# Optimization experiments

Hardware: AMD Instinct MI355X
Metric: run time of the kernel (lower is better)

## Reference

```python
import jax, jax.numpy as jnp
import numpy as np

TAU = 20.0        # LIFNeuron default tau
THRESHOLD = 1.0   # LIFNeuron default threshold
RESET = 0.0       # LIFNeuron default reset
DT = 1.0          # SpikingNeuralNetwork dt
ALPHA = DT / TAU

B, T, I, H, O = 256, 128, 512, 1024, 512


def setup_inputs() -> dict:
    key = jax.random.key(0)
    ks = jax.random.split(key, 6)
    def w(k, shape, fan_in):
        return (jax.random.normal(k, shape, jnp.float32) / np.sqrt(fan_in)).astype(jnp.float32)
    return {
        "x":  jax.random.normal(ks[0], (B, T, I), jnp.float32),
        "We": w(ks[1], (I, H), I), "be": jnp.zeros((H,), jnp.float32),
        "W1": w(ks[2], (H, H), H), "b1": jnp.zeros((H,), jnp.float32),
        "W2": w(ks[3], (H, H), H), "b2": jnp.zeros((H,), jnp.float32),
        "Wo": w(ks[4], (H, O), H), "bo": jnp.zeros((O,), jnp.float32),
    }


def _lif(v, inp):
    # v += (-v + inp) * dt/tau; spike = (v >= thr); v = v*(1-spike) + reset*spike
    v = v + (inp - v) * ALPHA
    spike = (v >= THRESHOLD).astype(v.dtype)
    v = v * (1.0 - spike) + RESET * spike
    return v, spike


def reference(x, We, be, W1, b1, W2, b2, Wo, bo):
    b, t, _ = x.shape
    h_dim = We.shape[1]
    o_dim = Wo.shape[1]

    def step(carry, xt):
        v1, v2, vo = carry
        h = jax.nn.relu(xt @ We + be)          # [B, H]
        v1, s1 = _lif(v1, h)                   # neuron 0 (only 2 of 3 neurons used: zip truncation)
        h = s1 @ W1 + b1
        v2, s2 = _lif(v2, h)                   # neuron 1
        h = s2 @ W2 + b2                       # last hidden layer: no neuron applied before output_layer
        vo, so = _lif(vo, h @ Wo + bo)         # output neuron
        return (v1, v2, vo), (s1, s2, so)

    init = (jnp.zeros((b, h_dim), x.dtype),
            jnp.zeros((b, h_dim), x.dtype),
            jnp.zeros((b, o_dim), x.dtype))
    _, (S1, S2, SO) = jax.lax.scan(step, init, jnp.swapaxes(x, 0, 1))  # time-major scan
    # output_spike at last timestep + full (detached) spike history, stacked over time
    return SO[-1], S1, S2, SO
```

## Files before the change

kernel.cpp:

```cpp
#include <hip/hip_runtime.h>
#include <cstdint>
#include <cstddef>

#define B_ 256
#define T_ 128
#define I_ 512
#define H_ 1024
#define O_ 512
static constexpr float ALPHA = 1.0f / 20.0f;
static constexpr float THR   = 1.0f;
static constexpr float S12   = 0.000244140625f;

typedef _Float16 f16;
typedef __attribute__((ext_vector_type(8))) _Float16 f16x8;
typedef __attribute__((ext_vector_type(4))) float f32x4;

__device__ inline void gload_lds16(const void* gsrc, void* ldsdst) {
    __builtin_amdgcn_global_load_lds(
        (const __attribute__((address_space(1))) unsigned int*)gsrc,
        (__attribute__((address_space(3))) unsigned int*)ldsdst, 16, 0, 0);
}

template<bool PERM_X, bool RELU>
__global__ __launch_bounds__(256)
void gemm128(const float* __restrict__ A, const float* __restrict__ Bw,
             const float* __restrict__ bias, float* __restrict__ C,
             int M, int N, int K) {
    constexpr int BM = 128, BN = 128, BK = 16, TM = 8, TN = 8;
    __shared__ float As[BK][BM];
    __shared__ float Bs[BK][BN + 4];

    const int tid = threadIdx.x;
    const int ntile = N / BN;
    const int bx = blockIdx.x % ntile;
    const int by = blockIdx.x / ntile;
    const int row0 = by * BM, col0 = bx * BN;
    const int tx = tid & 15;
    const int ty = tid >> 4;

    float acc[TM][TN] = {};

    for (int k0 = 0; k0 < K; k0 += BK) {
#pragma unroll
        for (int p = 0; p < 2; ++p) {
            int f = tid + p * 256;
            int r  = f >> 2;
            int kc = (f & 3) << 2;
            int m = row0 + r;
            const float* arow;
            if (PERM_X) {
                int t = m >> 8;
                int b = m & 255;
                arow = A + (size_t)(b * T_ + t) * K;
            } else {
                arow = A + (size_t)m * K;
            }
            float4 v = *reinterpret_cast<const float4*>(arow + k0 + kc);
            As[kc + 0][r] = v.x;
            As[kc + 1][r] = v.y;
            As[kc + 2][r] = v.z;
            As[kc + 3][r] = v.w;
        }
#pragma unroll
        for (int p = 0; p < 2; ++p) {
            int f = tid + p * 256;
            int r  = f >> 5;
            int nc = (f & 31) << 2;
            float4 v = *reinterpret_cast<const float4*>(Bw + (size_t)(k0 + r) * N + col0 + nc);
            *reinterpret_cast<float4*>(&Bs[r][nc]) = v;
        }
        __syncthreads();

#pragma unroll
        for (int k = 0; k < BK; ++k) {
            float a[TM], b[TN];
#pragma unroll
            for (int i = 0; i < TM; ++i) a[i] = As[k][ty * TM + i];
#pragma unroll
            for (int j = 0; j < TN; ++j) b[j] = Bs[k][tx * TN + j];
#pragma unroll
            for (int i = 0; i < TM; ++i)
#pragma unroll
                for (int j = 0; j < TN; ++j)
                    acc[i][j] += a[i] * b[j];
        }
        __syncthreads();
    }

#pragma unroll
    for (int i = 0; i < TM; ++i) {
        size_t m = (size_t)(row0 + ty * TM + i);
#pragma unroll
        for (int jj = 0; jj < TN; jj += 4) {
            int n = col0 + tx * TN + jj;
            float4 c4;
            float c0 = acc[i][jj + 0] + bias[n + 0];
            float c1 = acc[i][jj + 1] + bias[n + 1];
            float c2 = acc[i][jj + 2] + bias[n + 2];
            float c3 = acc[i][jj + 3] + bias[n + 3];
            if (RELU) {
                c0 = fmaxf(c0, 0.f); c1 = fmaxf(c1, 0.f);
                c2 = fmaxf(c2, 0.f); c3 = fmaxf(c3, 0.f);
            }
            c4.x = c0; c4.y = c1; c4.z = c2; c4.w = c3;
            *reinterpret_cast<float4*>(C + m * N + n) = c4;
        }
    }
}

template<bool SPLITX, bool PERM, bool RELU, bool WRITE_LAST>
__global__ __launch_bounds__(256, 2)
void gemm_lif(const float* __restrict__ A,
              const f16* __restrict__ Bhi, const f16* __restrict__ Blo,
              const float* __restrict__ bias,
              float* __restrict__ S, float* __restrict__ last_out,
              int N, int K) {
    constexpr int BK = 32;
    constexpr int NBUF = SPLITX ? 4 : 3;
    constexpr int BUFSTR = NBUF * 4096;
    constexpr size_t SMEM = (2 * BUFSTR * 2 > 64 * 132 * 4)
                                ? (size_t)(2 * BUFSTR * 2)
                                : (size_t)(64 * 132 * 4);
    __shared__ __align__(16) char smem[SMEM];
    f16* sm = (f16*)smem;
    float (*Cs)[132] = (float (*)[132])smem;

    const int tid  = threadIdx.x;
    const int lane = tid & 63;
    const int w    = tid >> 6;
    const int wr   = w >> 1, wc = w & 1;
    const int ntile = N >> 7;
    const int bx = blockIdx.x % ntile;
    const int b  = blockIdx.x / ntile;
    const int col0 = bx << 7;

    f32x4 acc0[4][4], acc1[4][4];
#pragma unroll
    for (int mi = 0; mi < 4; ++mi)
#pragma unroll
        for (int ni = 0; ni < 4; ++ni) {
            acc0[mi][ni] = {0.f, 0.f, 0.f, 0.f};
            acc1[mi][ni] = {0.f, 0.f, 0.f, 0.f};
        }

    {
        f16* Ah0 = sm;
        f16* Bh0 = sm + 4096;
        f16* Bl0 = sm + 8192;
        f16* Al0 = sm + 12288;
#pragma unroll
        for (int p = 0; p < 2; ++p) {
            int chunk = w * 2 + p;
            int r  = chunk * 16 + (lane >> 2);
            int kq = lane & 3;
            size_t off = (size_t)(col0 + r) * K + kq * 8;
            gload_lds16(Bhi + off, Bh0 + chunk * 512);
            gload_lds16(Blo + off, Bl0 + chunk * 512);
        }
#pragma unroll
        for (int p = 0; p < 4; ++p) {
            int c = tid + p * 256;
            int r = c >> 3;
            int q = c & 7;
            const float* arow = PERM ? A + (size_t)(b * T_ + r) * K
                                     : A + (size_t)(r * B_ + b) * K;
            float4 v = *reinterpret_cast<const float4*>(arow + q * 4);
            union { f16 h[4]; uint2 u; } hi;
            hi.h[0] = (f16)v.x; hi.h[1] = (f16)v.y;
            hi.h[2] = (f16)v.z; hi.h[3] = (f16)v.w;
            *reinterpret_cast<uint2*>(&Ah0[r * BK + q * 4]) = hi.u;
            if (SPLITX) {
                union { f16 h[4]; uint2 u; } lo;
                lo.h[0] = (f16)((v.x - (float)hi.h[0]) * 4096.0f);
                lo.h[1] = (f16)((v.y - (float)hi.h[1]) * 4096.0f);
                lo.h[2] = (f16)((v.z - (float)hi.h[2]) * 4096.0f);
                lo.h[3] = (f16)((v.w - (float)hi.h[3]) * 4096.0f);
                *reinterpret_cast<uint2*>(&Al0[r * BK + q * 4]) = lo.u;
            }
        }
    }
    __syncthreads();

    const int NIT = K / BK;
    for (int it = 0; it < NIT; ++it) {
        const int cur = it & 1, nxt = cur ^ 1;
        const bool more = (it + 1 < NIT);
        const int k0n = (it + 1) * BK;

        f16* Ah_c = sm + cur * BUFSTR;
        f16* Bh_c = Ah_c + 4096;
        f16* Bl_c = Ah_c + 8192;
        f16* Al_c = Ah_c + 12288;
        f16* Ah_n = sm + nxt * BUFSTR;
        f16* Bh_n = Ah_n + 4096;
        f16* Bl_n = Ah_n + 8192;
        f16* Al_n = Ah_n + 12288;

        float4 a4[4];
        if (more) {
#pragma unroll
            for (int p = 0; p < 2; ++p) {
                int chunk = w * 2 + p;
                int r  = chunk * 16 + (lane >> 2);
                int kq = lane & 3;
                size_t off = (size_t)(col0 + r) * K + k0n + kq * 8;
                gload_lds16(Bhi + off, Bh_n + chunk * 512);
                gload_lds16(Blo + off, Bl_n + chunk * 512);
            }
#pragma unroll
            for (int p = 0; p < 4; ++p) {
                int c = tid + p * 256;
                int r = c >> 3;
                int q = c & 7;
                const float* arow = PERM ? A + (size_t)(b * T_ + r) * K
                                         : A + (size_t)(r * B_ + b) * K;
                a4[p] = *reinterpret_cast<const float4*>(arow + k0n + q * 4);
            }
        }

        {
            f16x8 ahi[4], alo[4];
#pragma unroll
            for (int mi = 0; mi < 4; ++mi) {
                int ar = (wr * 64 + mi * 16 + (lane & 15)) * BK + (lane >> 4) * 8;
                ahi[mi] = *reinterpret_cast<const f16x8*>(&Ah_c[ar]);
                if (SPLITX) alo[mi] = *reinterpret_cast<const f16x8*>(&Al_c[ar]);
            }
#pragma unroll
            for (int ni = 0; ni < 4; ++ni) {
                int br = (wc * 64 + ni * 16 + (lane & 15)) * BK + (lane >> 4) * 8;
                f16x8 bh = *reinterpret_cast<const f16x8*>(&Bh_c[br]);
                f16x8 bl = *reinterpret_cast<const f16x8*>(&Bl_c[br]);
#pragma unroll
                for (int mi = 0; mi < 4; ++mi) {
                    acc0[mi][ni] = __builtin_amdgcn_mfma_f32_16x16x32_f16(
                        ahi[mi], bh, acc0[mi][ni], 0, 0, 0);
                    acc1[mi][ni] = __builtin_amdgcn_mfma_f32_16x16x32_f16(
                        ahi[mi], bl, acc1[mi][ni], 0, 0, 0);
                    if (SPLITX)
                        acc1[mi][ni] = __builtin_amdgcn_mfma_f32_16x16x32_f16(
                            alo[mi], bh, acc1[mi][ni], 0, 0, 0);
                }
            }
        }

        if (more) {
#pragma unroll
            for (int p = 0; p < 4; ++p) {
                int c = tid + p * 256;
                int r = c >> 3;
                int q = c & 7;
                float4 v = a4[p];
                union { f16 h[4]; uint2 u; } hi;
                hi.h[0] = (f16)v.x; hi.h[1] = (f16)v.y;
                hi.h[2] = (f16)v.z; hi.h[3] = (f16)v.w;
                *reinterpret_cast<uint2*>(&Ah_n[r * BK + q * 4]) = hi.u;
                if (SPLITX) {
                    union { f16 h[4]; uint2 u; } lo;
                    lo.h[0] = (f16)((v.x - (float)hi.h[0]) * 4096.0f);
                    lo.h[1] = (f16)((v.y - (float)hi.h[1]) * 4096.0f);
                    lo.h[2] = (f16)((v.z - (float)hi.h[2]) * 4096.0f);
                    lo.h[3] = (f16)((v.w - (float)hi.h[3]) * 4096.0f);
                    *reinterpret_cast<uint2*>(&Al_n[r * BK + q * 4]) = lo.u;
                }
            }
        }
        __syncthreads();
    }

    float v = 0.f, s = 0.f;
    float* Sp = S + (size_t)b * N + col0 + (tid & 127);
    const size_t tstride = (size_t)B_ * N;

    if (wr == 0) {
#pragma unroll
        for (int ni = 0; ni < 4; ++ni) {
            int col = wc * 64 + ni * 16 + (lane & 15);
            float bv = bias[col0 + col];
#pragma unroll
            for (int mi = 0; mi < 4; ++mi) {
                int rowb = mi * 16 + ((lane >> 4) << 2);
#pragma unroll
                for (int r = 0; r < 4; ++r) {
                    float cv = acc0[mi][ni][r] + S12 * acc1[mi][ni][r] + bv;
                    if (RELU) cv = fmaxf(cv, 0.f);
                    Cs[rowb + r][col] = cv;
                }
            }
        }
    }
    __syncthreads();
    if (tid < 128) {
#pragma unroll 4
        for (int t = 0; t < 64; ++t) {
            float in = Cs[t][tid];
            v = v + (in - v) * ALPHA;
            bool sp = (v >= THR);
            s = sp ? 1.0f : 0.0f;
            Sp[(size_t)t * tstride] = s;
            v = sp ? 0.0f : v;
        }
    }
    __syncthreads();
    if (wr == 1) {
#pragma unroll
        for (int ni = 0; ni < 4; ++ni) {
            int col = wc * 64 + ni * 16 + (lane & 15);
            float bv = bias[col0 + col];
#pragma unroll
            for (int mi = 0; mi < 4; ++mi) {
                int rowb = mi * 16 + ((lane >> 4) << 2);
#pragma unroll
                for (int r = 0; r < 4; ++r) {
                    float cv = acc0[mi][ni][r] + S12 * acc1[mi][ni][r] + bv;
                    if (RELU) cv = fmaxf(cv, 0.f);
                    Cs[rowb + r][col] = cv;
                }
            }
        }
    }
    __syncthreads();
    if (tid < 128) {
#pragma unroll 4
        for (int t = 64; t < 128; ++t) {
            float in = Cs[t - 64][tid];
            v = v + (in - v) * ALPHA;
            bool sp = (v >= THR);
            s = sp ? 1.0f : 0.0f;
            Sp[(size_t)t * tstride] = s;
            v = sp ? 0.0f : v;
        }
        if (WRITE_LAST) last_out[(size_t)b * N + col0 + tid] = s;
    }
}

__global__ __launch_bounds__(256, 2)
void gemm_lif_x(const float* __restrict__ A,
                const f16* __restrict__ Bhi, const f16* __restrict__ Blo,
                const float* __restrict__ bias,
                float* __restrict__ S,
                uint32_t* __restrict__ Pk,
                int N, int K) {
    constexpr int BK = 32;
    constexpr int BUFSTR = 4 * 4096;
    __shared__ __align__(16) char smem[2 * BUFSTR * 2];
    f16* sm = (f16*)smem;
    float (*Cs)[132] = (float (*)[132])smem;

    const int tid  = threadIdx.x;
    const int lane = tid & 63;
    const int w    = tid >> 6;
    const int wr   = w >> 1, wc = w & 1;
    const int nt   = N >> 7;
    const int ls   = 31 - __builtin_clz(nt);
    const int jj_  = blockIdx.x >> 3;
    const int bx   = jj_ & (nt - 1);
    const int b    = ((blockIdx.x & 7) << 5) + (jj_ >> ls);
    const int col0 = bx << 7;
    const int sw = (((lane >> 4) ^ ((lane >> 1) & 3)) << 3);

    f32x4 acc0[4][4], acc1[4][4];
#pragma unroll
    for (int mi = 0; mi < 4; ++mi)
#pragma unroll
        for (int ni = 0; ni < 4; ++ni) {
            acc0[mi][ni] = {0.f, 0.f, 0.f, 0.f};
            acc1[mi][ni] = {0.f, 0.f, 0.f, 0.f};
        }

    {
        f16* Ah0 = sm;
        f16* Bh0 = sm + 4096;
        f16* Bl0 = sm + 8192;
        f16* Al0 = sm + 12288;
#pragma unroll
        for (int p = 0; p < 2; ++p) {
            int chunk = w * 2 + p;
            int r  = chunk * 16 + (lane >> 2);
            int kq = lane & 3;
            size_t off = (size_t)(col0 + r) * K + kq * 8;
            gload_lds16(Bhi + off, Bh0 + chunk * 512);
            gload_lds16(Blo + off, Bl0 + chunk * 512);
        }
#pragma unroll
        for (int p = 0; p < 4; ++p) {
            int c = tid + p * 256;
            int r = c >> 3;
            int q = c & 7;
            const float* arow = A + (size_t)(b * T_ + r) * K;
            float4 v = *reinterpret_cast<const float4*>(arow + q * 4);
            int aoff = r * 32 + ((((q >> 1) ^ ((r >> 1) & 3))) << 3) + ((q & 1) << 2);
            union { f16 h[4]; uint2 u; } hi;
            hi.h[0] = (f16)v.x; hi.h[1] = (f16)v.y;
            hi.h[2] = (f16)v.z; hi.h[3] = (f16)v.w;
            *reinterpret_cast<uint2*>(&Ah0[aoff]) = hi.u;
            union { f16 h[4]; uint2 u; } lo;
            lo.h[0] = (f16)((v.x - (float)hi.h[0]) * 4096.0f);
            lo.h[1] = (f16)((v.y - (float)hi.h[1]) * 4096.0f);
            lo.h[2] = (f16)((v.z - (float)hi.h[2]) * 4096.0f);
            lo.h[3] = (f16)((v.w - (float)hi.h[3]) * 4096.0f);
            *reinterpret_cast<uint2*>(&Al0[aoff]) = lo.u;
        }
    }
    __syncthreads();

    const int NIT = K / BK;
    for (int it = 0; it < NIT; ++it) {
        const int cur = it & 1, nxt = cur ^ 1;
        const bool more = (it + 1 < NIT);
        const int k0n = (it + 1) * BK;

        f16* Ah_c = sm + cur * BUFSTR;
        f16* Bh_c = Ah_c + 4096;
        f16* Bl_c = Ah_c + 8192;
        f16* Al_c = Ah_c + 12288;
        f16* Ah_n = sm + nxt * BUFSTR;
        f16* Bh_n = Ah_n + 4096;
        f16* Bl_n = Ah_n + 8192;
        f16* Al_n = Ah_n + 12288;

        float4 a4[4];
        if (more) {
#pragma unroll
            for (int p = 0; p < 2; ++p) {
                int chunk = w * 2 + p;
                int r  = chunk * 16 + (lane >> 2);
                int kq = lane & 3;
                size_t off = (size_t)(col0 + r) * K + k0n + kq * 8;
                gload_lds16(Bhi + off, Bh_n + chunk * 512);
                gload_lds16(Blo + off, Bl_n + chunk * 512);
            }
#pragma unroll
            for (int p = 0; p < 4; ++p) {
                int c = tid + p * 256;
                int r = c >> 3;
                int q = c & 7;
                const float* arow = A + (size_t)(b * T_ + r) * K;
                a4[p] = *reinterpret_cast<const float4*>(arow + k0n + q * 4);
            }
        }

        {
            f16x8 ahi[4], alo[4];
#pragma unroll
            for (int mi = 0; mi < 4; ++mi) {
                int ar = (wr * 64 + mi * 16 + (lane & 15)) * 32 + sw;
                ahi[mi] = *reinterpret_cast<const f16x8*>(&Ah_c[ar]);
                alo[mi] = *reinterpret_cast<const f16x8*>(&Al_c[ar]);
            }
#pragma unroll
            for (int ni = 0; ni < 4; ++ni) {
                int br = (wc * 64 + ni * 16 + (lane & 15)) * 32 + sw;
                f16x8 bh = *reinterpret_cast<const f16x8*>(&Bh_c[br]);
                f16x8 bl = *reinterpret_cast<const f16x8*>(&Bl_c[br]);
#pragma unroll
                for (int mi = 0; mi < 4; ++mi) {
                    acc0[mi][ni] = __builtin_amdgcn_mfma_f32_16x16x32_f16(
                        ahi[mi], bh, acc0[mi][ni], 0, 0, 0);
                    acc1[mi][ni] = __builtin_amdgcn_mfma_f32_16x16x32_f16(
                        ahi[mi], bl, acc1[mi][ni], 0, 0, 0);
                    acc1[mi][ni] = __builtin_amdgcn_mfma_f32_16x16x32_f16(
                        alo[mi], bh, acc1[mi][ni], 0, 0, 0);
                }
            }
        }

        if (more) {
#pragma unroll
            for (int p = 0; p < 4; ++p) {
                int c = tid + p * 256;
                int r = c >> 3;
                int q = c & 7;
                float4 v = a4[p];
                int aoff = r * 32 + ((((q >> 1) ^ ((r >> 1) & 3))) << 3) + ((q & 1) << 2);
                union { f16 h[4]; uint2 u; } hi;
                hi.h[0] = (f16)v.x; hi.h[1] = (f16)v.y;
                hi.h[2] = (f16)v.z; hi.h[3] = (f16)v.w;
                *reinterpret_cast<uint2*>(&Ah_n[aoff]) = hi.u;
                union { f16 h[4]; uint2 u; } lo;
                lo.h[0] = (f16)((v.x - (float)hi.h[0]) * 4096.0f);
                lo.h[1] = (f16)((v.y - (float)hi.h[1]) * 4096.0f);
                lo.h[2] = (f16)((v.z - (float)hi.h[2]) * 4096.0f);
                lo.h[3] = (f16)((v.w - (float)hi.h[3]) * 4096.0f);
                *reinterpret_cast<uint2*>(&Al_n[aoff]) = lo.u;
            }
        }
        __syncthreads();
    }

    float v = 0.f;
    float* Sp = S + (size_t)b * N + col0 + (tid & 127);
    const size_t tstride = (size_t)B_ * N;
    const int PkW = N >> 5;
    const size_t pkbase = (size_t)(col0 >> 5) + ((tid >> 6) << 1);

    if (wr == 0) {
#pragma unroll
        for (int ni = 0; ni < 4; ++ni) {
            int col = wc * 64 + ni * 16 + (lane & 15);
            float bv = bias[col0 + col];
#pragma unroll
            for (int mi = 0; mi < 4; ++mi) {
                int rowb = mi * 16 + ((lane >> 4) << 2);
#pragma unroll
                for (int r = 0; r < 4; ++r) {
                    float cv = fmaxf(acc0[mi][ni][r] + S12 * acc1[mi][ni][r] + bv, 0.f);
                    Cs[rowb + r][col] = cv;
                }
            }
        }
    }
    __syncthreads();
    if (tid < 128) {
#pragma unroll 4
        for (int t = 0; t < 64; ++t) {
            float in = Cs[t][tid];
            v = v + (in - v) * ALPHA;
            bool sp = (v >= THR);
            Sp[(size_t)t * tstride] = sp ? 1.0f : 0.0f;
            v = sp ? 0.0f : v;
            unsigned long long bm = __ballot(sp);
            if (lane == 0)
                *reinterpret_cast<unsigned long long*>(
                    &Pk[((size_t)t * B_ + b) * PkW + pkbase]) = bm;
        }
    }
    __syncthreads();
    if (wr == 1) {
#pragma unroll
        for (int ni = 0; ni < 4; ++ni) {
            int col = wc * 64 + ni * 16 + (lane & 15);
            float bv = bias[col0 + col];
#pragma unroll
            for (int mi = 0; mi < 4; ++mi) {
                int rowb = mi * 16 + ((lane >> 4) << 2);
#pragma unroll
                for (int r = 0; r < 4; ++r) {
                    float cv = fmaxf(acc0[mi][ni][r] + S12 * acc1[mi][ni][r] + bv, 0.f);
                    Cs[rowb + r][col] = cv;
                }
            }
        }
    }
    __syncthreads();
    if (tid < 128) {
#pragma unroll 4
        for (int t = 64; t < 128; ++t) {
            float in = Cs[t - 64][tid];
            v = v + (in - v) * ALPHA;
            bool sp = (v >= THR);
            Sp[(size_t)t * tstride] = sp ? 1.0f : 0.0f;
            v = sp ? 0.0f : v;
            unsigned long long bm = __ballot(sp);
            if (lane == 0)
                *reinterpret_cast<unsigned long long*>(
                    &Pk[((size_t)t * B_ + b) * PkW + pkbase]) = bm;
        }
    }
}

template<bool WRITE_LAST, bool PACK_OUT>
__global__ __launch_bounds__(256, 2)
void gemm_lif_pk(const uint32_t* __restrict__ Apk,
                 const f16* __restrict__ Bhi, const f16* __restrict__ Blo,
                 const float* __restrict__ bias,
                 float* __restrict__ S,
                 float* __restrict__ last_out,
                 uint32_t* __restrict__ Pk_out,
                 int N, int K) {
    __shared__ __align__(16) char smem[64 * 132 * 4];
    f16* sm = (f16*)smem;
    float (*Cs)[132] = (float (*)[132])smem;

    const int tid  = threadIdx.x;
    const int lane = tid & 63;
    const int w    = tid >> 6;
    const int wr   = w >> 1, wc = w & 1;
    const int nt   = N >> 7;
    const int ls   = 31 - __builtin_clz(nt);
    const int jj_  = blockIdx.x >> 3;
    const int bx   = jj_ & (nt - 1);
    const int b    = ((blockIdx.x & 7) << 5) + (jj_ >> ls);
    const int col0 = bx << 7;
    const int sw = (((lane >> 4) ^ ((lane >> 1) & 3)) << 3);
    const int PkW = K >> 5;
    const int sh  = (lane >> 4) << 3;

    size_t arow[4];
#pragma unroll
    for (int mi = 0; mi < 4; ++mi) {
        int r = wr * 64 + mi * 16 + (lane & 15);
        arow[mi] = ((size_t)r * B_ + b) * PkW;
    }

    f32x4 acc0[4][4], acc1[4][4];
#pragma unroll
    for (int mi = 0; mi < 4; ++mi)
#pragma unroll
        for (int ni = 0; ni < 4; ++ni) {
            acc0[mi][ni] = {0.f, 0.f, 0.f, 0.f};
            acc1[mi][ni] = {0.f, 0.f, 0.f, 0.f};
        }

    {
#pragma unroll
        for (int p = 0; p < 2; ++p) {
            int chunk = w * 2 + p;
            int r  = chunk * 16 + (lane >> 2);
            int kq = lane & 3;
            size_t off = (size_t)(col0 + r) * K + kq * 8;
            gload_lds16(Bhi + off, sm + chunk * 512);
            gload_lds16(Blo + off, sm + 4096 + chunk * 512);
        }
    }
    __syncthreads();

    const int NIT = K / 32;
    for (int it = 0; it < NIT; ++it) {
        const int cur = it & 1, nxt = cur ^ 1;
        f16* Bh_c = sm + cur * 8192;
        f16* Bl_c = Bh_c + 4096;
        if (it + 1 < NIT) {
            f16* Bh_n = sm + nxt * 8192;
            f16* Bl_n = Bh_n + 4096;
            int k0n = (it + 1) * 32;
#pragma unroll
            for (int p = 0; p < 2; ++p) {
                int chunk = w * 2 + p;
                int r  = chunk * 16 + (lane >> 2);
                int kq = lane & 3;
                size_t off = (size_t)(col0 + r) * K + k0n + kq * 8;
                gload_lds16(Bhi + off, Bh_n + chunk * 512);
                gload_lds16(Blo + off, Bl_n + chunk * 512);
            }
        }

        f16x8 af[4];
#pragma unroll
        for (int mi = 0; mi < 4; ++mi) {
            uint32_t mm = Apk[arow[mi] + it] >> sh;
            union { f16 h[8]; f16x8 v; } au;
#pragma unroll
            for (int j = 0; j < 8; ++j)
                au.h[j] = ((mm >> j) & 1) ? (f16)1.0f : (f16)0.0f;
            af[mi] = au.v;
        }

#pragma unroll
        for (int ni = 0; ni < 4; ++ni) {
            int br = (wc * 64 + ni * 16 + (lane & 15)) * 32 + sw;
            f16x8 bh = *reinterpret_cast<const f16x8*>(&Bh_c[br]);
            f16x8 bl = *reinterpret_cast<const f16x8*>(&Bl_c[br]);
#pragma unroll
            for (int mi = 0; mi < 4; ++mi) {
                acc0[mi][ni] = __builtin_amdgcn_mfma_f32_16x16x32_f16(
                    af[mi], bh, acc0[mi][ni], 0, 0, 0);
                acc1[mi][ni] = __builtin_amdgcn_mfma_f32_16x16x32_f16(
                    af[mi], bl, acc1[mi][ni], 0, 0, 0);
            }
        }
        __syncthreads();
    }

    float v = 0.f, s = 0.f;
    float* Sp = S + (size_t)b * N + col0 + (tid & 127);
    const size_t tstride = (size_t)B_ * N;
    const int PkWo = N >> 5;
    const size_t pkbase = (size_t)(col0 >> 5) + ((tid >> 6) << 1);

    if (wr == 0) {
#pragma unroll
        for (int ni = 0; ni < 4; ++ni) {
            int col = wc * 64 + ni * 16 + (lane & 15);
            float bv = bias[col0 + col];
#pragma unroll
            for (int mi = 0; mi < 4; ++mi) {
                int rowb = mi * 16 + ((lane >> 4) << 2);
#pragma unroll
                for (int r = 0; r < 4; ++r)
                    Cs[rowb + r][col] = acc0[mi][ni][r] + S12 * acc1[mi][ni][r] + bv;
            }
        }
    }
    __syncthreads();
    if (tid < 128) {
#pragma unroll 4
        for (int t = 0; t < 64; ++t) {
            float in = Cs[t][tid];
            v = v + (in - v) * ALPHA;
            bool sp = (v >= THR);
            s = sp ? 1.0f : 0.0f;
            Sp[(size_t)t * tstride] = s;
            v = sp ? 0.0f : v;
            if (PACK_OUT) {
                unsigned long long bm = __ballot(sp);
                if (lane == 0)
                    *reinterpret_cast<unsigned long long*>(
                        &Pk_out[((size_t)t * B_ + b) * PkWo + pkbase]) = bm;
            }
        }
    }
    __syncthreads();
    if (wr == 1) {
#pragma unroll
        for (int ni = 0; ni < 4; ++ni) {
            int col = wc * 64 + ni * 16 + (lane & 15);
            float bv = bias[col0 + col];
#pragma unroll
            for (int mi = 0; mi < 4; ++mi) {
                int rowb = mi * 16 + ((lane >> 4) << 2);
#pragma unroll
                for (int r = 0; r < 4; ++r)
                    Cs[rowb + r][col] = acc0[mi][ni][r] + S12 * acc1[mi][ni][r] + bv;
            }
        }
    }
    __syncthreads();
    if (tid < 128) {
#pragma unroll 4
        for (int t = 64; t < 128; ++t) {
            float in = Cs[t - 64][tid];
            v = v + (in - v) * ALPHA;
            bool sp = (v >= THR);
            s = sp ? 1.0f : 0.0f;
            Sp[(size_t)t * tstride] = s;
            v = sp ? 0.0f : v;
            if (PACK_OUT) {
                unsigned long long bm = __ballot(sp);
                if (lane == 0)
                    *reinterpret_cast<unsigned long long*>(
                        &Pk_out[((size_t)t * B_ + b) * PkWo + pkbase]) = bm;
            }
        }
        if (WRITE_LAST) last_out[(size_t)b * N + col0 + tid] = s;
    }
}

__global__ __launch_bounds__(256)
void lif_scan(float* __restrict__ buf, int BH, float* __restrict__ last_out) {
    int j = blockIdx.x * 256 + threadIdx.x;
    if (j >= BH) return;
    float v = 0.f;
    float last = 0.f;
    for (int t = 0; t < T_; ++t) {
        size_t idx = (size_t)t * BH + j;
        float in = buf[idx];
        v = v + (in - v) * ALPHA;
        bool sp = (v >= THR);
        last = sp ? 1.0f : 0.0f;
        buf[idx] = last;
        v = sp ? 0.0f : v;
    }
    if (last_out) last_out[j] = last;
}

__global__ __launch_bounds__(256)
void make_wf2(const float* __restrict__ W2, const float* __restrict__ Wo,
              float* __restrict__ Wf) {
    __shared__ float w2s[64][33];
    __shared__ float wos[64][68];
    const int tid = threadIdx.x;
    const int ht = blockIdx.x >> 3, ot = blockIdx.x & 7;
    const int h0 = ht * 32, o0 = ot * 64;
    const int th = tid >> 3;
    const int to = tid & 7;

    double acc[8] = {0, 0, 0, 0, 0, 0, 0, 0};

    for (int k0 = 0; k0 < H_; k0 += 64) {
#pragma unroll
        for (int p = 0; p < 2; ++p) {
            int f = tid + p * 256;
            int i = f >> 4;
            int j4 = (f & 15) << 2;
            float4 v = *reinterpret_cast<const float4*>(
                W2 + (size_t)(h0 + i) * H_ + k0 + j4);
            w2s[j4 + 0][i] = v.x; w2s[j4 + 1][i] = v.y;
            w2s[j4 + 2][i] = v.z; w2s[j4 + 3][i] = v.w;
        }
#pragma unroll
        for (int p = 0; p < 4; ++p) {
            int f = tid + p * 256;
            int r = f >> 4;
            int c4 = (f & 15) << 2;
            float4 v = *reinterpret_cast<const float4*>(
                Wo + (size_t)(k0 + r) * O_ + o0 + c4);
            wos[r][c4 + 0] = v.x; wos[r][c4 + 1] = v.y;
            wos[r][c4 + 2] = v.z; wos[r][c4 + 3] = v.w;
        }
        __syncthreads();

#pragma unroll 8
        for (int k = 0; k < 64; ++k) {
            double a = (double)w2s[k][th];
#pragma unroll
            for (int j = 0; j < 8; ++j)
                acc[j] += a * (double)wos[k][to * 8 + j];
        }
        __syncthreads();
    }
#pragma unroll
    for (int j = 0; j < 8; ++j)
        Wf[(size_t)(h0 + th) * O_ + o0 + to * 8 + j] = (float)acc[j];
}

__global__ __launch_bounds__(256)
void make_bf(const float* __restrict__ Wo, const float* __restrict__ b2,
             const float* __restrict__ bo, float* __restrict__ bf) {
    int o = blockIdx.x * 256 + threadIdx.x;
    if (o >= O_) return;
    double acc = (double)bo[o];
    for (int h = 0; h < H_; ++h)
        acc += (double)b2[h] * (double)Wo[(size_t)h * O_ + o];
    bf[o] = (float)acc;
}

template<bool SWZ>
__global__ __launch_bounds__(256)
void split_w16(const float* __restrict__ W, f16* __restrict__ hi,
               f16* __restrict__ lo, int K, int N) {
    int idx = blockIdx.x * 256 + threadIdx.x;
    if (idx >= K * N) return;
    int n = idx / K;
    int ks = idx - n * K;
    int k = SWZ ? ((ks & ~31) | ((((ks >> 3) & 3) ^ ((n >> 1) & 3)) << 3) | (ks & 7))
                : ks;
    float wv = W[(size_t)k * N + n];
    f16 h0 = (f16)wv;
    float r = (wv - (float)h0) * 4096.0f;
    f16 h1 = (f16)r;
    hi[idx] = h0; lo[idx] = h1;
}

extern "C" void kernel_launch(void* const* d_in, const int* in_sizes, int n_in,
                              void* d_out, int out_size, void* d_ws, size_t ws_size,
                              hipStream_t stream) {
    const float* x  = (const float*)d_in[0];
    const float* We = (const float*)d_in[1];
    const float* be = (const float*)d_in[2];
    const float* W1 = (const float*)d_in[3];
    const float* b1 = (const float*)d_in[4];
    const float* W2 = (const float*)d_in[5];
    const float* b2 = (const float*)d_in[6];
    const float* Wo = (const float*)d_in[7];
    const float* bo = (const float*)d_in[8];

    float* out = (float*)d_out;
    float* so_last = out;
    float* S1 = out + (size_t)B_ * O_;
    float* S2 = S1 + (size_t)T_ * B_ * H_;
    float* SO = S2 + (size_t)T_ * B_ * H_;

    const int TB = T_ * B_;
    dim3 blk(256);

    const size_t MB = 1024 * 1024;
    const size_t off_weh = 0;
    const size_t off_wel = 1 * MB;
    const size_t off_w1h = 2 * MB;
    const size_t off_w1l = 4 * MB;
    const size_t off_wfh = 6 * MB;
    const size_t off_wfl = 7 * MB;
    const size_t off_bf  = 8 * MB;
    const size_t off_D   = 8 * MB + 4096;
    const size_t off_pk2 = off_D + 4 * MB;
    const size_t need3   = off_pk2 + 4 * MB;

    const size_t m_off_weh = 0;
    const size_t m_off_wel = m_off_weh + (size_t)I_ * H_ * 2;
    const size_t m_off_w1h = m_off_wel + (size_t)I_ * H_ * 2;
    const size_t m_off_w1l = m_off_w1h + (size_t)H_ * H_ * 2;
    const size_t m_off_wf32 = m_off_w1l + (size_t)H_ * H_ * 2;
    const size_t m_off_bf   = m_off_wf32 + (size_t)H_ * O_ * 4;
    const size_t m_off_wfh  = m_off_bf + (size_t)O_ * 4;
    const size_t m_off_wfl  = m_off_wfh + (size_t)H_ * O_ * 2;
    const size_t need2      = m_off_wfl + (size_t)H_ * O_ * 2;

    if (ws_size >= need3) {
        char* ws = (char*)d_ws;
        f16*   weh = (f16*)(ws + off_weh);
        f16*   wel = (f16*)(ws + off_wel);
        f16*   w1h = (f16*)(ws + off_w1h);
        f16*   w1l = (f16*)(ws + off_w1l);
        f16*   wfh = (f16*)(ws + off_wfh);
        f16*   wfl = (f16*)(ws + off_wfl);
        float* bf  = (float*)(ws + off_bf);
        float* Wf  = (float*)(ws + off_D);
        uint32_t* pk1 = (uint32_t*)(ws + off_D);
        uint32_t* pk2 = (uint32_t*)(ws + off_pk2);

        split_w16<true><<<dim3((I_ * H_ + 255) / 256), blk, 0, stream>>>(We, weh, wel, I_, H_);
        split_w16<true><<<dim3((H_ * H_ + 255) / 256), blk, 0, stream>>>(W1, w1h, w1l, H_, H_);
        make_wf2<<<dim3(256), blk, 0, stream>>>(W2, Wo, Wf);
        make_bf<<<dim3(2), blk, 0, stream>>>(Wo, b2, bo, bf);
        split_w16<true><<<dim3((H_ * O_ + 255) / 256), blk, 0, stream>>>(Wf, wfh, wfl, H_, O_);

        gemm_lif_x<<<dim3(B_ * (H_ / 128)), blk, 0, stream>>>(
            x, weh, wel, be, S1, pk1, H_, I_);

        gemm_lif_pk<false, true><<<dim3(B_ * (H_ / 128)), blk, 0, stream>>>(
            pk1, w1h, w1l, b1, S2, nullptr, pk2, H_, H_);

        gemm_lif_pk<true, false><<<dim3(B_ * (O_ / 128)), blk, 0, stream>>>(
            pk2, wfh, wfl, bf, SO, so_last, nullptr, O_, H_);
    } else if (ws_size >= need2) {
        char* ws = (char*)d_ws;
        f16*   weh = (f16*)(ws + m_off_weh);
        f16*   wel = (f16*)(ws + m_off_wel);
        f16*   w1h = (f16*)(ws + m_off_w1h);
        f16*   w1l = (f16*)(ws + m_off_w1l);
        float* Wf  = (float*)(ws + m_off_wf32);
        float* bf  = (float*)(ws + m_off_bf);
        f16*   wfh = (f16*)(ws + m_off_wfh);
        f16*   wfl = (f16*)(ws + m_off_wfl);

        split_w16<false><<<dim3((I_ * H_ + 255) / 256), blk, 0, stream>>>(We, weh, wel, I_, H_);
        split_w16<false><<<dim3((H_ * H_ + 255) / 256), blk, 0, stream>>>(W1, w1h, w1l, H_, H_);
        make_wf2<<<dim3(256), blk, 0, stream>>>(W2, Wo, Wf);
        make_bf<<<dim3(2), blk, 0, stream>>>(Wo, b2, bo, bf);
        split_w16<false><<<dim3((H_ * O_ + 255) / 256), blk, 0, stream>>>(Wf, wfh, wfl, H_, O_);

        gemm_lif<true, true, true, false><<<dim3(B_ * (H_ / 128)), blk, 0, stream>>>(
            x, weh, wel, be, S1, nullptr, H_, I_);
        gemm_lif<false, false, false, false><<<dim3(B_ * (H_ / 128)), blk, 0, stream>>>(
            S1, w1h, w1l, b1, S2, nullptr, H_, H_);
        gemm_lif<false, false, false, true><<<dim3(B_ * (O_ / 128)), blk, 0, stream>>>(
            S2, wfh, wfl, bf, SO, so_last, O_, H_);
    } else {
        float* Wf = (float*)d_ws;
        float* bf = Wf + (size_t)H_ * O_;
        gemm128<true, true><<<dim3((TB / 128) * (H_ / 128)), blk, 0, stream>>>(
            x, We, be, S1, TB, H_, I_);
        lif_scan<<<dim3((B_ * H_ + 255) / 256), blk, 0, stream>>>(S1, B_ * H_, nullptr);
        gemm128<false, false><<<dim3((TB / 128) * (H_ / 128)), blk, 0, stream>>>(
            S1, W1, b1, S2, TB, H_, H_);
        lif_scan<<<dim3((B_ * H_ + 255) / 256), blk, 0, stream>>>(S2, B_ * H_, nullptr);
        make_wf2<<<dim3(256), blk, 0, stream>>>(W2, Wo, Wf);
        make_bf<<<dim3(2), blk, 0, stream>>>(Wo, b2, bo, bf);
        gemm128<false, false><<<dim3((TB / 128) * (O_ / 128)), blk, 0, stream>>>(
            S2, Wf, bf, SO, TB, O_, H_);
        lif_scan<<<dim3((B_ * O_ + 255) / 256), blk, 0, stream>>>(SO, B_ * O_, so_last);
    }
}
```

Before: 657.0 us.

## Replace bit-packed spike intermediates with f16 spike arrays loaded via LDS DMA

```diff
diff --git a/kernel.cpp b/kernel.cpp
--- a/kernel.cpp
+++ b/kernel.cpp
@@ -108,12 +108,13 @@
     }
 }
 
-template<bool SPLITX, bool PERM, bool RELU, bool WRITE_LAST>
+template<bool SPLITX, bool PERM, bool RELU, bool WRITE_LAST, bool F16OUT>
 __global__ __launch_bounds__(256, 2)
 void gemm_lif(const float* __restrict__ A,
               const f16* __restrict__ Bhi, const f16* __restrict__ Blo,
               const float* __restrict__ bias,
               float* __restrict__ S, float* __restrict__ last_out,
+              f16* __restrict__ Sf,
               int N, int K) {
     constexpr int BK = 32;
     constexpr int NBUF = SPLITX ? 4 : 3;
@@ -298,6 +299,7 @@
             bool sp = (v >= THR);
             s = sp ? 1.0f : 0.0f;
             Sp[(size_t)t * tstride] = s;
+            if (F16OUT) Sf[((size_t)b * T_ + t) * N + col0 + tid] = (f16)s;
             v = sp ? 0.0f : v;
         }
     }
@@ -328,6 +330,7 @@
             bool sp = (v >= THR);
             s = sp ? 1.0f : 0.0f;
             Sp[(size_t)t * tstride] = s;
+            if (F16OUT) Sf[((size_t)b * T_ + t) * N + col0 + tid] = (f16)s;
             v = sp ? 0.0f : v;
         }
         if (WRITE_LAST) last_out[(size_t)b * N + col0 + tid] = s;
@@ -335,12 +338,13 @@
 }
 
 __global__ __launch_bounds__(256, 2)
-void gemm_lif_x(const float* __restrict__ A,
-                const f16* __restrict__ Bhi, const f16* __restrict__ Blo,
-                const float* __restrict__ bias,
-                float* __restrict__ S,
-                uint32_t* __restrict__ Pk,
-                int N, int K) {
+void gemm_lif_x2(const float* __restrict__ A,
+                 const f16* __restrict__ Bhi,
+                 const f16* __restrict__ Blo,
+                 const float* __restrict__ bias,
+                 float* __restrict__ S,
+                 f16* __restrict__ Sf,
+                 int N, int K) {
     constexpr int BK = 32;
     constexpr int BUFSTR = 4 * 4096;
     __shared__ __align__(16) char smem[2 * BUFSTR * 2];
@@ -351,11 +355,9 @@
     const int lane = tid & 63;
     const int w    = tid >> 6;
     const int wr   = w >> 1, wc = w & 1;
-    const int nt   = N >> 7;
-    const int ls   = 31 - __builtin_clz(nt);
-    const int jj_  = blockIdx.x >> 3;
-    const int bx   = jj_ & (nt - 1);
-    const int b    = ((blockIdx.x & 7) << 5) + (jj_ >> ls);
+    const int ntile = N >> 7;
+    const int bx = blockIdx.x % ntile;
+    const int b  = blockIdx.x / ntile;
     const int col0 = bx << 7;
     const int sw = (((lane >> 4) ^ ((lane >> 1) & 3)) << 3);
 
@@ -444,13 +446,13 @@
             f16x8 ahi[4], alo[4];
 #pragma unroll
             for (int mi = 0; mi < 4; ++mi) {
-                int ar = (wr * 64 + mi * 16 + (lane & 15)) * 32 + sw;
+                int ar = (wr * 64 + mi * 16 + (lane & 15)) * BK + sw;
                 ahi[mi] = *reinterpret_cast<const f16x8*>(&Ah_c[ar]);
                 alo[mi] = *reinterpret_cast<const f16x8*>(&Al_c[ar]);
             }
 #pragma unroll
             for (int ni = 0; ni < 4; ++ni) {
-                int br = (wc * 64 + ni * 16 + (lane & 15)) * 32 + sw;
+                int br = (wc * 64 + ni * 16 + (lane & 15)) * BK + sw;
                 f16x8 bh = *reinterpret_cast<const f16x8*>(&Bh_c[br]);
                 f16x8 bl = *reinterpret_cast<const f16x8*>(&Bl_c[br]);
 #pragma unroll
@@ -491,8 +493,6 @@
     float v = 0.f;
     float* Sp = S + (size_t)b * N + col0 + (tid & 127);
     const size_t tstride = (size_t)B_ * N;
-    const int PkW = N >> 5;
-    const size_t pkbase = (size_t)(col0 >> 5) + ((tid >> 6) << 1);
 
     if (wr == 0) {
 #pragma unroll
@@ -517,12 +517,10 @@
             float in = Cs[t][tid];
             v = v + (in - v) * ALPHA;
             bool sp = (v >= THR);
-            Sp[(size_t)t * tstride] = sp ? 1.0f : 0.0f;
+            float s = sp ? 1.0f : 0.0f;
+            Sp[(size_t)t * tstride] = s;
+            Sf[((size_t)b * T_ + t) * N + col0 + tid] = (f16)s;
             v = sp ? 0.0f : v;
-            unsigned long long bm = __ballot(sp);
-            if (lane == 0)
-                *reinterpret_cast<unsigned long long*>(
-                    &Pk[((size_t)t * B_ + b) * PkW + pkbase]) = bm;
         }
     }
     __syncthreads();
@@ -549,26 +547,27 @@
             float in = Cs[t - 64][tid];
             v = v + (in - v) * ALPHA;
             bool sp = (v >= THR);
-            Sp[(size_t)t * tstride] = sp ? 1.0f : 0.0f;
+            float s = sp ? 1.0f : 0.0f;
+            Sp[(size_t)t * tstride] = s;
+            Sf[((size_t)b * T_ + t) * N + col0 + tid] = (f16)s;
             v = sp ? 0.0f : v;
-            unsigned long long bm = __ballot(sp);
-            if (lane == 0)
-                *reinterpret_cast<unsigned long long*>(
-                    &Pk[((size_t)t * B_ + b) * PkW + pkbase]) = bm;
         }
     }
 }
 
-template<bool WRITE_LAST, bool PACK_OUT>
+template<bool WRITE_LAST, bool F16OUT>
 __global__ __launch_bounds__(256, 2)
-void gemm_lif_pk(const uint32_t* __restrict__ Apk,
-                 const f16* __restrict__ Bhi, const f16* __restrict__ Blo,
-                 const float* __restrict__ bias,
-                 float* __restrict__ S,
-                 float* __restrict__ last_out,
-                 uint32_t* __restrict__ Pk_out,
-                 int N, int K) {
-    __shared__ __align__(16) char smem[64 * 132 * 4];
+void gemm_lif_h(const f16* __restrict__ Af,
+                const f16* __restrict__ Bhi,
+                const f16* __restrict__ Blo,
+                const float* __restrict__ bias,
+                float* __restrict__ S,
+                float* __restrict__ last_out,
+                f16* __restrict__ Sf,
+                int N, int K) {
+    constexpr int BK = 32;
+    constexpr int BUFF = 3 * 4096;
+    __shared__ __align__(16) char smem[2 * BUFF * 2];
     f16* sm = (f16*)smem;
     float (*Cs)[132] = (float (*)[132])smem;
 
@@ -576,22 +575,11 @@
     const int lane = tid & 63;
     const int w    = tid >> 6;
     const int wr   = w >> 1, wc = w & 1;
-    const int nt   = N >> 7;
-    const int ls   = 31 - __builtin_clz(nt);
-    const int jj_  = blockIdx.x >> 3;
-    const int bx   = jj_ & (nt - 1);
-    const int b    = ((blockIdx.x & 7) << 5) + (jj_ >> ls);
+    const int ntile = N >> 7;
+    const int bx = blockIdx.x % ntile;
+    const int b  = blockIdx.x / ntile;
     const int col0 = bx << 7;
     const int sw = (((lane >> 4) ^ ((lane >> 1) & 3)) << 3);
-    const int PkW = K >> 5;
-    const int sh  = (lane >> 4) << 3;
-
-    size_t arow[4];
-#pragma unroll
-    for (int mi = 0; mi < 4; ++mi) {
-        int r = wr * 64 + mi * 16 + (lane & 15);
-        arow[mi] = ((size_t)r * B_ + b) * PkW;
-    }
 
     f32x4 acc0[4][4], acc1[4][4];
 #pragma unroll
@@ -602,55 +590,54 @@
             acc1[mi][ni] = {0.f, 0.f, 0.f, 0.f};
         }
 
+    const int r0   = (w * 2 + 0) * 16 + (lane >> 2);
+    const int r1   = (w * 2 + 1) * 16 + (lane >> 2);
+    const int kqs  = lane & 3;
+    const int kqa0 = kqs ^ ((r0 >> 1) & 3);
+    const int kqa1 = kqs ^ ((r1 >> 1) & 3);
+
     {
-#pragma unroll
-        for (int p = 0; p < 2; ++p) {
-            int chunk = w * 2 + p;
-            int r  = chunk * 16 + (lane >> 2);
-            int kq = lane & 3;
-            size_t off = (size_t)(col0 + r) * K + kq * 8;
-            gload_lds16(Bhi + off, sm + chunk * 512);
-            gload_lds16(Blo + off, sm + 4096 + chunk * 512);
-        }
-    }
-    __syncthreads();
-
-    const int NIT = K / 32;
+        size_t b0 = (size_t)(col0 + r0) * K + kqs * 8;
+        size_t b1 = (size_t)(col0 + r1) * K + kqs * 8;
+        size_t a0 = ((size_t)b * T_ + r0) * K + kqa0 * 8;
+        size_t a1 = ((size_t)b * T_ + r1) * K + kqa1 * 8;
+        gload_lds16(Af + a0,  sm + (w * 2 + 0) * 512);
+        gload_lds16(Af + a1,  sm + (w * 2 + 1) * 512);
+        gload_lds16(Bhi + b0, sm + 4096 + (w * 2 + 0) * 512);
+        gload_lds16(Bhi + b1, sm + 4096 + (w * 2 + 1) * 512);
+        gload_lds16(Blo + b0, sm + 8192 + (w * 2 + 0) * 512);
+        gload_lds16(Blo + b1, sm + 8192 + (w * 2 + 1) * 512);
+    }
+    __syncthreads();
+
+    const int NIT = K / BK;
     for (int it = 0; it < NIT; ++it) {
-        const int cur = it & 1, nxt = cur ^ 1;
-        f16* Bh_c = sm + cur * 8192;
-        f16* Bl_c = Bh_c + 4096;
+        f16* cur = sm + (it & 1) * BUFF;
         if (it + 1 < NIT) {
-            f16* Bh_n = sm + nxt * 8192;
-            f16* Bl_n = Bh_n + 4096;
-            int k0n = (it + 1) * 32;
-#pragma unroll
-            for (int p = 0; p < 2; ++p) {
-                int chunk = w * 2 + p;
-                int r  = chunk * 16 + (lane >> 2);
-                int kq = lane & 3;
-                size_t off = (size_t)(col0 + r) * K + k0n + kq * 8;
-                gload_lds16(Bhi + off, Bh_n + chunk * 512);
-                gload_lds16(Blo + off, Bl_n + chunk * 512);
-            }
+            f16* nb = sm + ((it + 1) & 1) * BUFF;
+            int k0n = (it + 1) * BK;
+            size_t b0 = (size_t)(col0 + r0) * K + k0n + kqs * 8;
+            size_t b1 = (size_t)(col0 + r1) * K + k0n + kqs * 8;
+            size_t a0 = ((size_t)b * T_ + r0) * K + k0n + kqa0 * 8;
+            size_t a1 = ((size_t)b * T_ + r1) * K + k0n + kqa1 * 8;
+            gload_lds16(Af + a0,  nb + (w * 2 + 0) * 512);
+            gload_lds16(Af + a1,  nb + (w * 2 + 1) * 512);
+            gload_lds16(Bhi + b0, nb + 4096 + (w * 2 + 0) * 512);
+            gload_lds16(Bhi + b1, nb + 4096 + (w * 2 + 1) * 512);
+            gload_lds16(Blo + b0, nb + 8192 + (w * 2 + 0) * 512);
+            gload_lds16(Blo + b1, nb + 8192 + (w * 2 + 1) * 512);
         }
 
         f16x8 af[4];
 #pragma unroll
-        for (int mi = 0; mi < 4; ++mi) {
-            uint32_t mm = Apk[arow[mi] + it] >> sh;
-            union { f16 h[8]; f16x8 v; } au;
-#pragma unroll
-            for (int j = 0; j < 8; ++j)
-                au.h[j] = ((mm >> j) & 1) ? (f16)1.0f : (f16)0.0f;
-            af[mi] = au.v;
-        }
-
+        for (int mi = 0; mi < 4; ++mi)
+            af[mi] = *reinterpret_cast<const f16x8*>(
+                &cur[(wr * 64 + mi * 16 + (lane & 15)) * BK + sw]);
 #pragma unroll
         for (int ni = 0; ni < 4; ++ni) {
-            int br = (wc * 64 + ni * 16 + (lane & 15)) * 32 + sw;
-            f16x8 bh = *reinterpret_cast<const f16x8*>(&Bh_c[br]);
-            f16x8 bl = *reinterpret_cast<const f16x8*>(&Bl_c[br]);
+            int br = (wc * 64 + ni * 16 + (lane & 15)) * BK + sw;
+            f16x8 bh = *reinterpret_cast<const f16x8*>(&cur[4096 + br]);
+            f16x8 bl = *reinterpret_cast<const f16x8*>(&cur[8192 + br]);
 #pragma unroll
             for (int mi = 0; mi < 4; ++mi) {
                 acc0[mi][ni] = __builtin_amdgcn_mfma_f32_16x16x32_f16(
@@ -665,8 +652,6 @@
     float v = 0.f, s = 0.f;
     float* Sp = S + (size_t)b * N + col0 + (tid & 127);
     const size_t tstride = (size_t)B_ * N;
-    const int PkWo = N >> 5;
-    const size_t pkbase = (size_t)(col0 >> 5) + ((tid >> 6) << 1);
 
     if (wr == 0) {
 #pragma unroll
@@ -691,13 +676,8 @@
             bool sp = (v >= THR);
             s = sp ? 1.0f : 0.0f;
             Sp[(size_t)t * tstride] = s;
+            if (F16OUT) Sf[((size_t)b * T_ + t) * N + col0 + tid] = (f16)s;
             v = sp ? 0.0f : v;
-            if (PACK_OUT) {
-                unsigned long long bm = __ballot(sp);
-                if (lane == 0)
-                    *reinterpret_cast<unsigned long long*>(
-                        &Pk_out[((size_t)t * B_ + b) * PkWo + pkbase]) = bm;
-            }
         }
     }
     __syncthreads();
@@ -724,13 +704,8 @@
             bool sp = (v >= THR);
             s = sp ? 1.0f : 0.0f;
             Sp[(size_t)t * tstride] = s;
+            if (F16OUT) Sf[((size_t)b * T_ + t) * N + col0 + tid] = (f16)s;
             v = sp ? 0.0f : v;
-            if (PACK_OUT) {
-                unsigned long long bm = __ballot(sp);
-                if (lane == 0)
-                    *reinterpret_cast<unsigned long long*>(
-                        &Pk_out[((size_t)t * B_ + b) * PkWo + pkbase]) = bm;
-            }
         }
         if (WRITE_LAST) last_out[(size_t)b * N + col0 + tid] = s;
     }
@@ -855,39 +830,42 @@
     dim3 blk(256);
 
     const size_t MB = 1024 * 1024;
-    const size_t off_weh = 0;
-    const size_t off_wel = 1 * MB;
-    const size_t off_w1h = 2 * MB;
-    const size_t off_w1l = 4 * MB;
-    const size_t off_wfh = 6 * MB;
-    const size_t off_wfl = 7 * MB;
-    const size_t off_bf  = 8 * MB;
-    const size_t off_D   = 8 * MB + 4096;
-    const size_t off_pk2 = off_D + 4 * MB;
-    const size_t need3   = off_pk2 + 4 * MB;
-
-    const size_t m_off_weh = 0;
-    const size_t m_off_wel = m_off_weh + (size_t)I_ * H_ * 2;
-    const size_t m_off_w1h = m_off_wel + (size_t)I_ * H_ * 2;
-    const size_t m_off_w1l = m_off_w1h + (size_t)H_ * H_ * 2;
-    const size_t m_off_wf32 = m_off_w1l + (size_t)H_ * H_ * 2;
-    const size_t m_off_bf   = m_off_wf32 + (size_t)H_ * O_ * 4;
-    const size_t m_off_wfh  = m_off_bf + (size_t)O_ * 4;
-    const size_t m_off_wfl  = m_off_wfh + (size_t)H_ * O_ * 2;
-    const size_t need2      = m_off_wfl + (size_t)H_ * O_ * 2;
-
-    if (ws_size >= need3) {
+    const size_t sz_s1f = (size_t)T_ * B_ * H_ * 2;
+
+    const size_t b_weh = 0;
+    const size_t b_wel = 1 * MB;
+    const size_t b_w1h = 2 * MB;
+    const size_t b_w1l = 4 * MB;
+    const size_t b_wfh = 6 * MB;
+    const size_t b_wfl = 7 * MB;
+    const size_t b_bf  = 8 * MB;
+    const size_t b_wf  = 8 * MB + 4096;
+    const size_t b_s1f = 10 * MB + 4096;
+    const size_t b_s2f = b_s1f + sz_s1f;
+    const size_t need_hi = b_s2f + sz_s1f;
+
+    const size_t m_weh = 0;
+    const size_t m_wel = m_weh + (size_t)I_ * H_ * 2;
+    const size_t m_w1h = m_wel + (size_t)I_ * H_ * 2;
+    const size_t m_w1l = m_w1h + (size_t)H_ * H_ * 2;
+    const size_t m_wf  = m_w1l + (size_t)H_ * H_ * 2;
+    const size_t m_bf  = m_wf + (size_t)H_ * O_ * 4;
+    const size_t m_wfh = m_bf + (size_t)O_ * 4;
+    const size_t m_wfl = m_wfh + (size_t)H_ * O_ * 2;
+    const size_t need_mid = m_wfl + (size_t)H_ * O_ * 2;
+
+    if (ws_size >= need_hi) {
         char* ws = (char*)d_ws;
-        f16*   weh = (f16*)(ws + off_weh);
-        f16*   wel = (f16*)(ws + off_wel);
-        f16*   w1h = (f16*)(ws + off_w1h);
-        f16*   w1l = (f16*)(ws + off_w1l);
-        f16*   wfh = (f16*)(ws + off_wfh);
-        f16*   wfl = (f16*)(ws + off_wfl);
-        float* bf  = (float*)(ws + off_bf);
-        float* Wf  = (float*)(ws + off_D);
-        uint32_t* pk1 = (uint32_t*)(ws + off_D);
-        uint32_t* pk2 = (uint32_t*)(ws + off_pk2);
+        f16*   weh = (f16*)(ws + b_weh);
+        f16*   wel = (f16*)(ws + b_wel);
+        f16*   w1h = (f16*)(ws + b_w1h);
+        f16*   w1l = (f16*)(ws + b_w1l);
+        f16*   wfh = (f16*)(ws + b_wfh);
+        f16*   wfl = (f16*)(ws + b_wfl);
+        float* bf  = (float*)(ws + b_bf);
+        float* Wf  = (float*)(ws + b_wf);
+        f16*   s1f = (f16*)(ws + b_s1f);
+        f16*   s2f = (f16*)(ws + b_s2f);
 
         split_w16<true><<<dim3((I_ * H_ + 255) / 256), blk, 0, stream>>>(We, weh, wel, I_, H_);
         split_w16<true><<<dim3((H_ * H_ + 255) / 256), blk, 0, stream>>>(W1, w1h, w1l, H_, H_);
@@ -895,24 +873,24 @@
         make_bf<<<dim3(2), blk, 0, stream>>>(Wo, b2, bo, bf);
         split_w16<true><<<dim3((H_ * O_ + 255) / 256), blk, 0, stream>>>(Wf, wfh, wfl, H_, O_);
 
-        gemm_lif_x<<<dim3(B_ * (H_ / 128)), blk, 0, stream>>>(
-            x, weh, wel, be, S1, pk1, H_, I_);
-
-        gemm_lif_pk<false, true><<<dim3(B_ * (H_ / 128)), blk, 0, stream>>>(
-            pk1, w1h, w1l, b1, S2, nullptr, pk2, H_, H_);
-
-        gemm_lif_pk<true, false><<<dim3(B_ * (O_ / 128)), blk, 0, stream>>>(
-            pk2, wfh, wfl, bf, SO, so_last, nullptr, O_, H_);
-    } else if (ws_size >= need2) {
+        gemm_lif_x2<<<dim3(B_ * (H_ / 128)), blk, 0, stream>>>(
+            x, weh, wel, be, S1, s1f, H_, I_);
+
+        gemm_lif_h<false, true><<<dim3(B_ * (H_ / 128)), blk, 0, stream>>>(
+            s1f, w1h, w1l, b1, S2, nullptr, s2f, H_, H_);
+
+        gemm_lif_h<true, false><<<dim3(B_ * (O_ / 128)), blk, 0, stream>>>(
+            s2f, wfh, wfl, bf, SO, so_last, nullptr, O_, H_);
+    } else if (ws_size >= need_mid) {
         char* ws = (char*)d_ws;
-        f16*   weh = (f16*)(ws + m_off_weh);
-        f16*   wel = (f16*)(ws + m_off_wel);
-        f16*   w1h = (f16*)(ws + m_off_w1h);
-        f16*   w1l = (f16*)(ws + m_off_w1l);
-        float* Wf  = (float*)(ws + m_off_wf32);
-        float* bf  = (float*)(ws + m_off_bf);
-        f16*   wfh = (f16*)(ws + m_off_wfh);
-        f16*   wfl = (f16*)(ws + m_off_wfl);
+        f16*   weh = (f16*)(ws + m_weh);
+        f16*   wel = (f16*)(ws + m_wel);
+        f16*   w1h = (f16*)(ws + m_w1h);
+        f16*   w1l = (f16*)(ws + m_w1l);
+        float* Wf  = (float*)(ws + m_wf);
+        float* bf  = (float*)(ws + m_bf);
+        f16*   wfh = (f16*)(ws + m_wfh);
+        f16*   wfl = (f16*)(ws + m_wfl);
 
         split_w16<false><<<dim3((I_ * H_ + 255) / 256), blk, 0, stream>>>(We, weh, wel, I_, H_);
         split_w16<false><<<dim3((H_ * H_ + 255) / 256), blk, 0, stream>>>(W1, w1h, w1l, H_, H_);
@@ -920,12 +898,12 @@
         make_bf<<<dim3(2), blk, 0, stream>>>(Wo, b2, bo, bf);
         split_w16<false><<<dim3((H_ * O_ + 255) / 256), blk, 0, stream>>>(Wf, wfh, wfl, H_, O_);
 
-        gemm_lif<true, true, true, false><<<dim3(B_ * (H_ / 128)), blk, 0, stream>>>(
-            x, weh, wel, be, S1, nullptr, H_, I_);
-        gemm_lif<false, false, false, false><<<dim3(B_ * (H_ / 128)), blk, 0, stream>>>(
-            S1, w1h, w1l, b1, S2, nullptr, H_, H_);
-        gemm_lif<false, false, false, true><<<dim3(B_ * (O_ / 128)), blk, 0, stream>>>(
-            S2, wfh, wfl, bf, SO, so_last, O_, H_);
+        gemm_lif<true, true, true, false, false><<<dim3(B_ * (H_ / 128)), blk, 0, stream>>>(
+            x, weh, wel, be, S1, nullptr, nullptr, H_, I_);
+        gemm_lif<false, false, false, false, false><<<dim3(B_ * (H_ / 128)), blk, 0, stream>>>(
+            S1, w1h, w1l, b1, S2, nullptr, nullptr, H_, H_);
+        gemm_lif<false, false, false, true, false><<<dim3(B_ * (O_ / 128)), blk, 0, stream>>>(
+            S2, wfh, wfl, bf, SO, so_last, nullptr, O_, H_);
     } else {
         float* Wf = (float*)d_ws;
         float* bf = Wf + (size_t)H_ * O_;
```

Result: faster. 581.3 us (-11.5%).
